# Performance work log

Measured on AMD Instinct MI355X. Metric: run time of the kernel, lower is better.

The kernel has to match this reference:

```python
import jax, jax.numpy as jnp
import numpy as np

N_NODES = 50000
N_EDGES = 800000
D = 64


def setup_inputs() -> dict:
    key = jax.random.key(0)
    ks = jax.random.split(key, 8)
    x = jax.random.normal(ks[0], (N_NODES, D), dtype=jnp.float32)
    edge_index = jax.random.randint(ks[1], (2, N_EDGES), 0, N_NODES, dtype=jnp.int64)
    # GCNConv params (PyG: Linear without bias inside lin, bias added after aggregation)
    def glorot(k, fan_in, fan_out):
        lim = (6.0 / (fan_in + fan_out)) ** 0.5
        return jax.random.uniform(k, (fan_in, fan_out), jnp.float32, -lim, lim)
    W1 = glorot(ks[2], D, D); b1 = jnp.zeros((D,), jnp.float32)
    W2 = glorot(ks[3], D, D); b2 = jnp.zeros((D,), jnp.float32)
    W3 = glorot(ks[4], D, D); b3 = jnp.zeros((D,), jnp.float32)
    return {"x": x, "edge_index": edge_index,
            "W1": W1, "b1": b1, "W2": W2, "b2": b2, "W3": W3, "b3": b3}


def _gcn_norm(edge_index, n_nodes, dtype):
    # Add self-loops, compute symmetric normalization D^-1/2 (A+I) D^-1/2 (PyG GCNConv default).
    loop = jnp.arange(n_nodes, dtype=edge_index.dtype)
    src = jnp.concatenate([edge_index[0], loop])  # message source j
    dst = jnp.concatenate([edge_index[1], loop])  # aggregation target i
    deg = jax.ops.segment_sum(jnp.ones_like(dst, dtype=dtype), dst, num_segments=n_nodes)
    dinv = jnp.where(deg > 0, jax.lax.rsqrt(deg), 0.0)
    norm = dinv[src] * dinv[dst]  # [E + N]
    return src, dst, norm


def _gcn_conv(x, src, dst, norm, W, b, n_nodes):
    h = x @ W                              # [N, D_out]
    msg = h[src] * norm[:, None]           # gather + scale, [E+N, D_out]
    out = jax.ops.segment_sum(msg, dst, num_segments=n_nodes)  # scatter-add
    return out + b


def reference(x, edge_index, W1, b1, W2, b2, W3, b3):
    n = x.shape[0]
    src, dst, norm = _gcn_norm(edge_index, n, x.dtype)
    # layer 0: conv -> relu -> residual
    h = _gcn_conv(x, src, dst, norm, W1, b1, n)
    h = jax.nn.relu(h) + x
    # layer 1: conv -> relu -> residual
    r = h
    h = _gcn_conv(h, src, dst, norm, W2, b2, n)
    h = jax.nn.relu(h) + r
    # layer 2 (final): conv only
    h = _gcn_conv(h, src, dst, norm, W3, b3, n)
    return h
```

## Files before the change

### kernel.cpp

```cpp
#include <hip/hip_runtime.h>
#include <hip/hip_bf16.h>


#define CAP 64
#define EDGE_CHUNK 1024

typedef __attribute__((ext_vector_type(8))) short bf16x8;
typedef __attribute__((ext_vector_type(4))) float f32x4;

__device__ inline unsigned pack_bf16(float a, float b) {
    union { float f; unsigned i; } ua, ub;
    ua.f = a; ub.f = b;
    unsigned x = (ua.i + 0x7fffu + ((ua.i >> 16) & 1u)) >> 16;
    unsigned y = (ub.i + 0x7fffu + ((ub.i >> 16) & 1u)) >> 16;
    return x | (y << 16);
}
__device__ inline unsigned short to_bf16(float a) {
    union { float f; unsigned i; } u; u.f = a;
    return (unsigned short)((u.i + 0x7fffu + ((u.i >> 16) & 1u)) >> 16);
}
__device__ inline void acc_bf16x2(unsigned u, float& a, float& b) {
    union { unsigned i; float f; } lo, hi;
    lo.i = u << 16;
    hi.i = u & 0xffff0000u;
    a += lo.f; b += hi.f;
}

__global__ void fill_kernel(const int* __restrict__ src, const int* __restrict__ dst,
                            int* __restrict__ cnt, int* __restrict__ adj,
                            int E, int npc) {
    int cls = blockIdx.x & 7;
    int base = (blockIdx.x >> 3) * EDGE_CHUNK;
    int end = min(base + EDGE_CHUNK, E);
    int lo = cls * npc, hi = lo + npc;
    for (int e = base + threadIdx.x; e < end; e += blockDim.x) {
        int d = dst[e];
        if (d >= lo && d < hi) {
            int p = atomicAdd(&cnt[d], 1);
            adj[(size_t)d * CAP + p] = src[e];
        }
    }
}

__global__ __launch_bounds__(256) void gemm_kernel(const float* __restrict__ in,
                                                   const float* __restrict__ W,
                                                   const int* __restrict__ cnt,
                                                   unsigned short* __restrict__ g, int n) {
    __shared__ unsigned short Wb[512 * 8];
    int t = threadIdx.x;

#pragma unroll
    for (int e0 = 0; e0 < 2; e0++) {
        int e = t + e0 * 256;
        int sc = e >> 6;
        int l  = e & 63;
        int s = sc >> 2, c = sc & 3;
        int nn = c * 16 + (l & 15);
        int kb = s * 32 + (l >> 4) * 8;
        const float* wp = &W[(size_t)kb * 64 + nn];
        unsigned q0 = pack_bf16(wp[0 * 64], wp[1 * 64]);
        unsigned q1 = pack_bf16(wp[2 * 64], wp[3 * 64]);
        unsigned q2 = pack_bf16(wp[4 * 64], wp[5 * 64]);
        unsigned q3 = pack_bf16(wp[6 * 64], wp[7 * 64]);
        *(uint4*)&Wb[e * 8] = make_uint4(q0, q1, q2, q3);
    }

    int wv = t >> 6;
    int lane = t & 63;
    int quad = lane >> 4;
    int m16 = lane & 15;

    int rowA = blockIdx.x * 64 + wv * 16 + m16;
    union { bf16x8 v; uint4 u; } a0, a1;
    {
        float4 f0 = make_float4(0, 0, 0, 0), f1 = f0, f2 = f0, f3 = f0;
        if (rowA < n) {
            const float* rp = &in[(size_t)rowA * 64];
            f0 = *(const float4*)&rp[quad * 8];
            f1 = *(const float4*)&rp[quad * 8 + 4];
            f2 = *(const float4*)&rp[32 + quad * 8];
            f3 = *(const float4*)&rp[32 + quad * 8 + 4];
        }
        a0.u = make_uint4(pack_bf16(f0.x, f0.y), pack_bf16(f0.z, f0.w),
                          pack_bf16(f1.x, f1.y), pack_bf16(f1.z, f1.w));
        a1.u = make_uint4(pack_bf16(f2.x, f2.y), pack_bf16(f2.z, f2.w),
                          pack_bf16(f3.x, f3.y), pack_bf16(f3.z, f3.w));
    }
    __syncthreads();

    f32x4 acc[4];
#pragma unroll
    for (int c = 0; c < 4; c++) {
        bf16x8 b0 = *(const bf16x8*)&Wb[((size_t)(0 * 4 + c) * 64 + lane) * 8];
        bf16x8 b1 = *(const bf16x8*)&Wb[((size_t)(1 * 4 + c) * 64 + lane) * 8];
        f32x4 z = {0.f, 0.f, 0.f, 0.f};
        z = __builtin_amdgcn_mfma_f32_16x16x32_bf16(a0.v, b0, z, 0, 0, 0);
        z = __builtin_amdgcn_mfma_f32_16x16x32_bf16(a1.v, b1, z, 0, 0, 0);
        acc[c] = z;
    }

    int rowbase = blockIdx.x * 64 + wv * 16 + quad * 4;
    float dv[4];
#pragma unroll
    for (int r = 0; r < 4; r++) {
        int row = rowbase + r;
        dv[r] = (row < n) ? rsqrtf((float)(cnt[row] + 1)) : 0.f;
    }
#pragma unroll
    for (int c = 0; c < 4; c++) {
#pragma unroll
        for (int r = 0; r < 4; r++) {
            int row = rowbase + r;
            if (row < n)
                g[(size_t)row * 64 + c * 16 + m16] = to_bf16(acc[c][r] * dv[r]);
        }
    }
}

template <int MODE>
__global__ __launch_bounds__(256) void agg_kernel(const unsigned short* __restrict__ g,
                                                  const int* __restrict__ cnt,
                                                  const int* __restrict__ adj,
                                                  const float* __restrict__ bias,
                                                  const float* __restrict__ res,
                                                  float* __restrict__ out, int n) {
    int t = threadIdx.x;
    int lg = t & 15;
    int i = blockIdx.x * 16 + (t >> 4);
    if (i >= n) return;
    int deg = cnt[i];
    const int* lst = adj + (size_t)i * CAP;
    const int c4 = lg * 4;
    float ax = 0.f, ay = 0.f, az = 0.f, aw = 0.f;
    {
        uint2 v = *(const uint2*)&g[(size_t)i * 64 + c4];
        acc_bf16x2(v.x, ax, ay);
        acc_bf16x2(v.y, az, aw);
    }
    int k = 0;
    for (; k + 8 <= deg; k += 8) {
        int j0 = lst[k], j1 = lst[k + 1], j2 = lst[k + 2], j3 = lst[k + 3];
        int j4 = lst[k + 4], j5 = lst[k + 5], j6 = lst[k + 6], j7 = lst[k + 7];
        uint2 v0 = *(const uint2*)&g[(size_t)j0 * 64 + c4];
        uint2 v1 = *(const uint2*)&g[(size_t)j1 * 64 + c4];
        uint2 v2 = *(const uint2*)&g[(size_t)j2 * 64 + c4];
        uint2 v3 = *(const uint2*)&g[(size_t)j3 * 64 + c4];
        uint2 v4 = *(const uint2*)&g[(size_t)j4 * 64 + c4];
        uint2 v5 = *(const uint2*)&g[(size_t)j5 * 64 + c4];
        uint2 v6 = *(const uint2*)&g[(size_t)j6 * 64 + c4];
        uint2 v7 = *(const uint2*)&g[(size_t)j7 * 64 + c4];
        acc_bf16x2(v0.x, ax, ay); acc_bf16x2(v0.y, az, aw);
        acc_bf16x2(v1.x, ax, ay); acc_bf16x2(v1.y, az, aw);
        acc_bf16x2(v2.x, ax, ay); acc_bf16x2(v2.y, az, aw);
        acc_bf16x2(v3.x, ax, ay); acc_bf16x2(v3.y, az, aw);
        acc_bf16x2(v4.x, ax, ay); acc_bf16x2(v4.y, az, aw);
        acc_bf16x2(v5.x, ax, ay); acc_bf16x2(v5.y, az, aw);
        acc_bf16x2(v6.x, ax, ay); acc_bf16x2(v6.y, az, aw);
        acc_bf16x2(v7.x, ax, ay); acc_bf16x2(v7.y, az, aw);
    }
    if (k + 4 <= deg) {
        int j0 = lst[k], j1 = lst[k + 1], j2 = lst[k + 2], j3 = lst[k + 3];
        uint2 v0 = *(const uint2*)&g[(size_t)j0 * 64 + c4];
        uint2 v1 = *(const uint2*)&g[(size_t)j1 * 64 + c4];
        uint2 v2 = *(const uint2*)&g[(size_t)j2 * 64 + c4];
        uint2 v3 = *(const uint2*)&g[(size_t)j3 * 64 + c4];
        acc_bf16x2(v0.x, ax, ay); acc_bf16x2(v0.y, az, aw);
        acc_bf16x2(v1.x, ax, ay); acc_bf16x2(v1.y, az, aw);
        acc_bf16x2(v2.x, ax, ay); acc_bf16x2(v2.y, az, aw);
        acc_bf16x2(v3.x, ax, ay); acc_bf16x2(v3.y, az, aw);
        k += 4;
    }
    for (; k < deg; k++) {
        uint2 v = *(const uint2*)&g[(size_t)lst[k] * 64 + c4];
        acc_bf16x2(v.x, ax, ay);
        acc_bf16x2(v.y, az, aw);
    }
    float dv = rsqrtf((float)(deg + 1));
    float4 bb = *(const float4*)&bias[c4];
    float4 v;
    v.x = dv * ax + bb.x;
    v.y = dv * ay + bb.y;
    v.z = dv * az + bb.z;
    v.w = dv * aw + bb.w;
    if (MODE == 0) {
        float4 r = *(const float4*)&res[(size_t)i * 64 + c4];
        v.x = fmaxf(v.x, 0.f) + r.x;
        v.y = fmaxf(v.y, 0.f) + r.y;
        v.z = fmaxf(v.z, 0.f) + r.z;
        v.w = fmaxf(v.w, 0.f) + r.w;
    }
    *(float4*)&out[(size_t)i * 64 + c4] = v;
}

extern "C" void kernel_launch(void* const* d_in, const int* in_sizes, int n_in,
                              void* d_out, int out_size, void* d_ws, size_t ws_size,
                              hipStream_t stream) {
    const float* x  = (const float*)d_in[0];
    const int*   ei = (const int*)d_in[1];
    const float* W1 = (const float*)d_in[2];
    const float* b1 = (const float*)d_in[3];
    const float* W2 = (const float*)d_in[4];
    const float* b2 = (const float*)d_in[5];
    const float* W3 = (const float*)d_in[6];
    const float* b3 = (const float*)d_in[7];
    float* out = (float*)d_out;

    const int N = in_sizes[0] / 64;
    const int E = in_sizes[1] / 2;
    const int* src = ei;
    const int* dst = ei + E;
    const int npc = (N + 7) / 8;
    const int nEdgeChunks = (E + EDGE_CHUNK - 1) / EDGE_CHUNK;

    char* p = (char*)d_ws;
    int*            cnt = (int*)p;            p += ((N + 63) / 64) * 64 * 4;
    int*            adj = (int*)p;            p += ((size_t)N + 1) * CAP * 4;
    unsigned short* g   = (unsigned short*)p; p += (size_t)N * 64 * 2;
    float*          h   = (float*)p;          p += (size_t)N * 64 * 4;

    const int aggBlocks  = (N + 15) / 16;
    const int gemmBlocks = (N + 63) / 64;

    hipMemsetAsync(cnt, 0, (size_t)N * 4, stream);
    fill_kernel<<<nEdgeChunks * 8, 256, 0, stream>>>(src, dst, cnt, adj, E, npc);

    gemm_kernel<<<gemmBlocks, 256, 0, stream>>>(x, W1, cnt, g, N);
    agg_kernel<0><<<aggBlocks, 256, 0, stream>>>(g, cnt, adj, b1, x, h, N);

    gemm_kernel<<<gemmBlocks, 256, 0, stream>>>(h, W2, cnt, g, N);
    agg_kernel<0><<<aggBlocks, 256, 0, stream>>>(g, cnt, adj, b2, h, h, N);

    gemm_kernel<<<gemmBlocks, 256, 0, stream>>>(h, W3, cnt, g, N);
    agg_kernel<1><<<aggBlocks, 256, 0, stream>>>(g, cnt, adj, b3, nullptr, out, N);
}
```

Baseline: 198.6 us.

## Split bf16 feature table into two column planes and aggregate each separately

The GEMM now writes its bf16 output as two 32-column planes, each N×32. Each aggregation becomes two launches, one per plane. The idea is that each gather pass touches a 3.2MB working set instead of 6.4MB, so more of it stays resident in L2/MALL cache during random neighbor gathers. The cost is that the adjacency lists and degrees are read twice, there are more kernel launches, and each gathered row segment is a smaller 64B access.

```diff
diff --git a/kernel.cpp b/kernel.cpp
--- a/kernel.cpp
+++ b/kernel.cpp
@@ -106,34 +106,38 @@
         int row = rowbase + r;
         dv[r] = (row < n) ? rsqrtf((float)(cnt[row] + 1)) : 0.f;
     }
+    size_t pstride = (size_t)n * 32;
 #pragma unroll
     for (int c = 0; c < 4; c++) {
+        unsigned short* gp = g + (size_t)(c >> 1) * pstride;
+        int colp = (c & 1) * 16 + m16;
 #pragma unroll
         for (int r = 0; r < 4; r++) {
             int row = rowbase + r;
             if (row < n)
-                g[(size_t)row * 64 + c * 16 + m16] = to_bf16(acc[c][r] * dv[r]);
+                gp[(size_t)row * 32 + colp] = to_bf16(acc[c][r] * dv[r]);
         }
     }
 }
 
 template <int MODE>
-__global__ __launch_bounds__(256) void agg_kernel(const unsigned short* __restrict__ g,
+__global__ __launch_bounds__(256) void agg_kernel(const unsigned short* __restrict__ gplane,
                                                   const int* __restrict__ cnt,
                                                   const int* __restrict__ adj,
                                                   const float* __restrict__ bias,
                                                   const float* __restrict__ res,
-                                                  float* __restrict__ out, int n) {
+                                                  float* __restrict__ out,
+                                                  int co, int n) {
     int t = threadIdx.x;
-    int lg = t & 15;
-    int i = blockIdx.x * 16 + (t >> 4);
+    int lg = t & 7;
+    int i = blockIdx.x * 32 + (t >> 3);
     if (i >= n) return;
     int deg = cnt[i];
     const int* lst = adj + (size_t)i * CAP;
     const int c4 = lg * 4;
     float ax = 0.f, ay = 0.f, az = 0.f, aw = 0.f;
     {
-        uint2 v = *(const uint2*)&g[(size_t)i * 64 + c4];
+        uint2 v = *(const uint2*)&gplane[(size_t)i * 32 + c4];
         acc_bf16x2(v.x, ax, ay);
         acc_bf16x2(v.y, az, aw);
     }
@@ -141,14 +145,14 @@
     for (; k + 8 <= deg; k += 8) {
         int j0 = lst[k], j1 = lst[k + 1], j2 = lst[k + 2], j3 = lst[k + 3];
         int j4 = lst[k + 4], j5 = lst[k + 5], j6 = lst[k + 6], j7 = lst[k + 7];
-        uint2 v0 = *(const uint2*)&g[(size_t)j0 * 64 + c4];
-        uint2 v1 = *(const uint2*)&g[(size_t)j1 * 64 + c4];
-        uint2 v2 = *(const uint2*)&g[(size_t)j2 * 64 + c4];
-        uint2 v3 = *(const uint2*)&g[(size_t)j3 * 64 + c4];
-        uint2 v4 = *(const uint2*)&g[(size_t)j4 * 64 + c4];
-        uint2 v5 = *(const uint2*)&g[(size_t)j5 * 64 + c4];
-        uint2 v6 = *(const uint2*)&g[(size_t)j6 * 64 + c4];
-        uint2 v7 = *(const uint2*)&g[(size_t)j7 * 64 + c4];
+        uint2 v0 = *(const uint2*)&gplane[(size_t)j0 * 32 + c4];
+        uint2 v1 = *(const uint2*)&gplane[(size_t)j1 * 32 + c4];
+        uint2 v2 = *(const uint2*)&gplane[(size_t)j2 * 32 + c4];
+        uint2 v3 = *(const uint2*)&gplane[(size_t)j3 * 32 + c4];
+        uint2 v4 = *(const uint2*)&gplane[(size_t)j4 * 32 + c4];
+        uint2 v5 = *(const uint2*)&gplane[(size_t)j5 * 32 + c4];
+        uint2 v6 = *(const uint2*)&gplane[(size_t)j6 * 32 + c4];
+        uint2 v7 = *(const uint2*)&gplane[(size_t)j7 * 32 + c4];
         acc_bf16x2(v0.x, ax, ay); acc_bf16x2(v0.y, az, aw);
         acc_bf16x2(v1.x, ax, ay); acc_bf16x2(v1.y, az, aw);
         acc_bf16x2(v2.x, ax, ay); acc_bf16x2(v2.y, az, aw);
@@ -160,10 +164,10 @@
     }
     if (k + 4 <= deg) {
         int j0 = lst[k], j1 = lst[k + 1], j2 = lst[k + 2], j3 = lst[k + 3];
-        uint2 v0 = *(const uint2*)&g[(size_t)j0 * 64 + c4];
-        uint2 v1 = *(const uint2*)&g[(size_t)j1 * 64 + c4];
-        uint2 v2 = *(const uint2*)&g[(size_t)j2 * 64 + c4];
-        uint2 v3 = *(const uint2*)&g[(size_t)j3 * 64 + c4];
+        uint2 v0 = *(const uint2*)&gplane[(size_t)j0 * 32 + c4];
+        uint2 v1 = *(const uint2*)&gplane[(size_t)j1 * 32 + c4];
+        uint2 v2 = *(const uint2*)&gplane[(size_t)j2 * 32 + c4];
+        uint2 v3 = *(const uint2*)&gplane[(size_t)j3 * 32 + c4];
         acc_bf16x2(v0.x, ax, ay); acc_bf16x2(v0.y, az, aw);
         acc_bf16x2(v1.x, ax, ay); acc_bf16x2(v1.y, az, aw);
         acc_bf16x2(v2.x, ax, ay); acc_bf16x2(v2.y, az, aw);
@@ -171,7 +175,7 @@
         k += 4;
     }
     for (; k < deg; k++) {
-        uint2 v = *(const uint2*)&g[(size_t)lst[k] * 64 + c4];
+        uint2 v = *(const uint2*)&gplane[(size_t)lst[k] * 32 + c4];
         acc_bf16x2(v.x, ax, ay);
         acc_bf16x2(v.y, az, aw);
     }
@@ -182,14 +186,15 @@
     v.y = dv * ay + bb.y;
     v.z = dv * az + bb.z;
     v.w = dv * aw + bb.w;
+    size_t rowoff = (size_t)i * 64 + co + c4;
     if (MODE == 0) {
-        float4 r = *(const float4*)&res[(size_t)i * 64 + c4];
+        float4 r = *(const float4*)&res[rowoff];
         v.x = fmaxf(v.x, 0.f) + r.x;
         v.y = fmaxf(v.y, 0.f) + r.y;
         v.z = fmaxf(v.z, 0.f) + r.z;
         v.w = fmaxf(v.w, 0.f) + r.w;
     }
-    *(float4*)&out[(size_t)i * 64 + c4] = v;
+    *(float4*)&out[rowoff] = v;
 }
 
 extern "C" void kernel_launch(void* const* d_in, const int* in_sizes, int n_in,
@@ -217,19 +222,25 @@
     int*            adj = (int*)p;            p += ((size_t)N + 1) * CAP * 4;
     unsigned short* g   = (unsigned short*)p; p += (size_t)N * 64 * 2;
     float*          h   = (float*)p;          p += (size_t)N * 64 * 4;
-
-    const int aggBlocks  = (N + 15) / 16;
+    const size_t pstride = (size_t)N * 32;
+    unsigned short* g0 = g;
+    unsigned short* g1 = g + pstride;
+
+    const int aggBlocks  = (N + 31) / 32;
     const int gemmBlocks = (N + 63) / 64;
 
     hipMemsetAsync(cnt, 0, (size_t)N * 4, stream);
     fill_kernel<<<nEdgeChunks * 8, 256, 0, stream>>>(src, dst, cnt, adj, E, npc);
 
     gemm_kernel<<<gemmBlocks, 256, 0, stream>>>(x, W1, cnt, g, N);
-    agg_kernel<0><<<aggBlocks, 256, 0, stream>>>(g, cnt, adj, b1, x, h, N);
+    agg_kernel<0><<<aggBlocks, 256, 0, stream>>>(g0, cnt, adj, b1,      x, h, 0,  N);
+    agg_kernel<0><<<aggBlocks, 256, 0, stream>>>(g1, cnt, adj, b1 + 32, x, h, 32, N);
 
     gemm_kernel<<<gemmBlocks, 256, 0, stream>>>(h, W2, cnt, g, N);
-    agg_kernel<0><<<aggBlocks, 256, 0, stream>>>(g, cnt, adj, b2, h, h, N);
+    agg_kernel<0><<<aggBlocks, 256, 0, stream>>>(g0, cnt, adj, b2,      h, h, 0,  N);
+    agg_kernel<0><<<aggBlocks, 256, 0, stream>>>(g1, cnt, adj, b2 + 32, h, h, 32, N);
 
     gemm_kernel<<<gemmBlocks, 256, 0, stream>>>(h, W3, cnt, g, N);
-    agg_kernel<1><<<aggBlocks, 256, 0, stream>>>(g, cnt, adj, b3, nullptr, out, N);
-}
+    agg_kernel<1><<<aggBlocks, 256, 0, stream>>>(g0, cnt, adj, b3,      nullptr, out, 0,  N);
+    agg_kernel<1><<<aggBlocks, 256, 0, stream>>>(g1, cnt, adj, b3 + 32, nullptr, out, 32, N);
+}
```

Measured after the change: 213.8 us. 1.08x slower.

## Sort nodes by in-degree into bins so aggregation groups balance work

Applied to the files above, without the earlier changes.

Adds a histogram, scan and placement pass that builds a permutation of nodes ordered by in-degree (counting sort over 64 bins). The aggregation kernels then process nodes in this order, so each 16-node block and wavefront handles nodes with similar degree and less time is lost to divergence and imbalance. The cost is three extra small kernel launches plus an indirection through perm, and output writes become scattered rather than row-contiguous.

```diff
diff --git a/kernel.cpp b/kernel.cpp
--- a/kernel.cpp
+++ b/kernel.cpp
@@ -40,6 +40,49 @@
             adj[(size_t)d * CAP + p] = src[e];
         }
     }
+}
+
+__global__ void hist_kernel(const int* __restrict__ cnt, int* __restrict__ hist, int n) {
+    __shared__ int lh[64];
+    int t = threadIdx.x;
+    if (t < 64) lh[t] = 0;
+    __syncthreads();
+    int i = blockIdx.x * blockDim.x + t;
+    if (i < n) atomicAdd(&lh[min(cnt[i], 63)], 1);
+    __syncthreads();
+    if (t < 64 && lh[t]) atomicAdd(&hist[t], lh[t]);
+}
+
+__global__ void binscan_kernel(const int* __restrict__ hist, int* __restrict__ binpos) {
+    int lane = threadIdx.x & 63;
+    int v = hist[lane];
+    int orig = v;
+#pragma unroll
+    for (int off = 1; off < 64; off <<= 1) {
+        int u = __shfl_up(v, off);
+        if (lane >= off) v += u;
+    }
+    binpos[lane] = v - orig;
+}
+
+__global__ void place_kernel(const int* __restrict__ cnt, int* __restrict__ binpos,
+                             int* __restrict__ perm, int n) {
+    __shared__ int lh[64];
+    __shared__ int lbase[64];
+    int t = threadIdx.x;
+    if (t < 64) lh[t] = 0;
+    __syncthreads();
+    int i = blockIdx.x * blockDim.x + t;
+    int d = 0, lp = 0;
+    bool ok = (i < n);
+    if (ok) {
+        d = min(cnt[i], 63);
+        lp = atomicAdd(&lh[d], 1);
+    }
+    __syncthreads();
+    if (t < 64) lbase[t] = lh[t] ? atomicAdd(&binpos[t], lh[t]) : 0;
+    __syncthreads();
+    if (ok) perm[lbase[d] + lp] = i;
 }
 
 __global__ __launch_bounds__(256) void gemm_kernel(const float* __restrict__ in,
@@ -121,13 +164,15 @@
 __global__ __launch_bounds__(256) void agg_kernel(const unsigned short* __restrict__ g,
                                                   const int* __restrict__ cnt,
                                                   const int* __restrict__ adj,
+                                                  const int* __restrict__ perm,
                                                   const float* __restrict__ bias,
                                                   const float* __restrict__ res,
                                                   float* __restrict__ out, int n) {
     int t = threadIdx.x;
     int lg = t & 15;
-    int i = blockIdx.x * 16 + (t >> 4);
-    if (i >= n) return;
+    int slot = blockIdx.x * 16 + (t >> 4);
+    if (slot >= n) return;
+    int i = perm[slot];
     int deg = cnt[i];
     const int* lst = adj + (size_t)i * CAP;
     const int c4 = lg * 4;
@@ -211,25 +256,33 @@
     const int* dst = ei + E;
     const int npc = (N + 7) / 8;
     const int nEdgeChunks = (E + EDGE_CHUNK - 1) / EDGE_CHUNK;
+    const int cntSlots = ((N + 63) / 64) * 64;
 
     char* p = (char*)d_ws;
-    int*            cnt = (int*)p;            p += ((N + 63) / 64) * 64 * 4;
-    int*            adj = (int*)p;            p += ((size_t)N + 1) * CAP * 4;
-    unsigned short* g   = (unsigned short*)p; p += (size_t)N * 64 * 2;
-    float*          h   = (float*)p;          p += (size_t)N * 64 * 4;
+    int*            cnt    = (int*)p;            p += (size_t)cntSlots * 4;
+    int*            hist   = (int*)p;            p += 64 * 4;
+    int*            binpos = (int*)p;            p += 64 * 4;
+    int*            perm   = (int*)p;            p += (size_t)N * 4;
+    int*            adj    = (int*)p;            p += ((size_t)N + 1) * CAP * 4;
+    unsigned short* g      = (unsigned short*)p; p += (size_t)N * 64 * 2;
+    float*          h      = (float*)p;          p += (size_t)N * 64 * 4;
 
     const int aggBlocks  = (N + 15) / 16;
     const int gemmBlocks = (N + 63) / 64;
-
-    hipMemsetAsync(cnt, 0, (size_t)N * 4, stream);
+    const int nBlocks    = (N + 255) / 256;
+
+    hipMemsetAsync(cnt, 0, ((size_t)cntSlots + 128) * 4, stream);
     fill_kernel<<<nEdgeChunks * 8, 256, 0, stream>>>(src, dst, cnt, adj, E, npc);
+    hist_kernel<<<nBlocks, 256, 0, stream>>>(cnt, hist, N);
+    binscan_kernel<<<1, 64, 0, stream>>>(hist, binpos);
+    place_kernel<<<nBlocks, 256, 0, stream>>>(cnt, binpos, perm, N);
 
     gemm_kernel<<<gemmBlocks, 256, 0, stream>>>(x, W1, cnt, g, N);
-    agg_kernel<0><<<aggBlocks, 256, 0, stream>>>(g, cnt, adj, b1, x, h, N);
+    agg_kernel<0><<<aggBlocks, 256, 0, stream>>>(g, cnt, adj, perm, b1, x, h, N);
 
     gemm_kernel<<<gemmBlocks, 256, 0, stream>>>(h, W2, cnt, g, N);
-    agg_kernel<0><<<aggBlocks, 256, 0, stream>>>(g, cnt, adj, b2, h, h, N);
+    agg_kernel<0><<<aggBlocks, 256, 0, stream>>>(g, cnt, adj, perm, b2, h, h, N);
 
     gemm_kernel<<<gemmBlocks, 256, 0, stream>>>(h, W3, cnt, g, N);
-    agg_kernel<1><<<aggBlocks, 256, 0, stream>>>(g, cnt, adj, b3, nullptr, out, N);
-}
+    agg_kernel<1><<<aggBlocks, 256, 0, stream>>>(g, cnt, adj, perm, b3, nullptr, out, N);
+}
```

Result: slower. 225.3 us (+13.4%).
